# Performance work log

Measured on AMD Instinct MI355X. Metric: run time of the kernel, lower is better.

## Reference

```python
import jax, jax.numpy as jnp
import numpy as np

B, T, D, H = 4, 2048, 1024, 16
DK = D // H

def setup_inputs() -> dict:
    key = jax.random.key(0)
    ks = jax.random.split(key, 5)
    s = 1.0 / np.sqrt(D)
    return {
        "x": jax.random.normal(ks[0], (B, T, D), jnp.float32),
        "Wq": jax.random.normal(ks[1], (D, D), jnp.float32) * s,
        "Wk": jax.random.normal(ks[2], (D, D), jnp.float32) * s,
        "Wv": jax.random.normal(ks[3], (D, D), jnp.float32) * s,
        "Wo": jax.random.normal(ks[4], (D, D), jnp.float32) * s,
    }

def reference(x, Wq, Wk, Wv, Wo):
    # torch Linear: y = x @ W.T (W is [out, in], no bias)
    q = jnp.einsum('btd,ed->bte', x, Wq).reshape(B, T, H, DK).transpose(0, 2, 1, 3)
    k = jnp.einsum('btd,ed->bte', x, Wk).reshape(B, T, H, DK).transpose(0, 2, 1, 3)
    v = jnp.einsum('btd,ed->bte', x, Wv).reshape(B, T, H, DK).transpose(0, 2, 1, 3)
    # scores: [B, H, T, T]
    scores = jnp.einsum('bhqd,bhkd->bhqk', q, k) * (DK ** -0.5)
    causal_mask = jnp.triu(jnp.ones((T, T), dtype=bool), k=1)  # True above diagonal
    scores = jnp.where(causal_mask, -jnp.inf, scores)
    attn = jax.nn.softmax(scores, axis=-1)  # dropout = identity (p=0 / eval)
    ctx = jnp.einsum('bhqk,bhkd->bhqd', attn, v)  # [B, H, T, DK]
    ctx = ctx.transpose(0, 2, 1, 3).reshape(B, T, D)
    out = jnp.einsum('btd,ed->bte', ctx, Wo)
    return out
```

## Files before the change

### kernel.cpp

```cpp
#include <hip/hip_runtime.h>
#include <hip/hip_bf16.h>
#include <stdint.h>

#define BB 4
#define TT 2048
#define DD 1024
#define HH 16
#define DKK 64

typedef unsigned short u16;
typedef unsigned int u32;
typedef __bf16 bf16_t;
typedef bf16_t bf16x8 __attribute__((ext_vector_type(8)));
typedef float f32x4 __attribute__((ext_vector_type(4)));

#if __has_builtin(__builtin_amdgcn_exp2f)
#define EXPW(x) __builtin_amdgcn_exp2f(x)
#define QSCL 0.1803368801111244f
#else
#define EXPW(x) __expf(x)
#define QSCL 0.125f
#endif

__device__ __forceinline__ float bf2f(u16 u) {
    u32 x = ((u32)u) << 16;
    float f;
    __builtin_memcpy(&f, &x, 4);
    return f;
}
__device__ __forceinline__ u16 f2bf(float f) {
    u32 x;
    __builtin_memcpy(&x, &f, 4);
    x += 0x7fffu + ((x >> 16) & 1u);
    return (u16)(x >> 16);
}

__device__ __forceinline__ void gll16(const u16* g, u16* l) {
    __builtin_amdgcn_global_load_lds((const __attribute__((address_space(1))) u32*)g,
                                     (__attribute__((address_space(3))) u32*)l, 16, 0, 0);
}

__global__ void cast_f32_bf16(const float* __restrict__ in, u16* __restrict__ out, int n) {
    int i = (blockIdx.x * blockDim.x + threadIdx.x) * 4;
    int stride = gridDim.x * blockDim.x * 4;
    for (; i < n; i += stride) {
        float4 v = *reinterpret_cast<const float4*>(in + i);
        uint2 pk;
        pk.x = (u32)f2bf(v.x) | ((u32)f2bf(v.y) << 16);
        pk.y = (u32)f2bf(v.z) | ((u32)f2bf(v.w) << 16);
        *reinterpret_cast<uint2*>(out + i) = pk;
    }
}

__global__ void cast_w4(const float* __restrict__ w0, const float* __restrict__ w1,
                        const float* __restrict__ w2, const float* __restrict__ w3,
                        u16* __restrict__ out, int nW) {
    const float* src = (blockIdx.y == 0) ? w0 : (blockIdx.y == 1) ? w1 : (blockIdx.y == 2) ? w2 : w3;
    u16* dst = out + (size_t)blockIdx.y * nW;
    int i = (blockIdx.x * blockDim.x + threadIdx.x) * 4;
    int stride = gridDim.x * blockDim.x * 4;
    for (; i < nW; i += stride) {
        float4 v = *reinterpret_cast<const float4*>(src + i);
        uint2 pk;
        pk.x = (u32)f2bf(v.x) | ((u32)f2bf(v.y) << 16);
        pk.y = (u32)f2bf(v.z) | ((u32)f2bf(v.w) << 16);
        *reinterpret_cast<uint2*>(dst + i) = pk;
    }
}

__device__ __forceinline__ void gemm_128_mainloop(const u16* __restrict__ A,
                                                  const u16* __restrict__ W,
                                                  u16* As, u16* Bs,
                                                  int m0, int n0, f32x4 acc[4][4]) {
    const int tid = threadIdx.x;
    const int lane = tid & 63;
    const int wid = tid >> 6;
    const int wr = (wid >> 1) * 64, wc = (wid & 1) * 64;
    const int l15 = lane & 15, l4 = lane >> 4;

    const f32x4 z4 = {0.f, 0.f, 0.f, 0.f};
#pragma unroll
    for (int i = 0; i < 4; i++)
#pragma unroll
        for (int j = 0; j < 4; j++) acc[i][j] = z4;

    const int r0 = tid >> 2;
    const int c0 = (tid & 3) * 8;

    for (int k0 = 0; k0 < DD; k0 += 32) {
        __syncthreads();
        gll16(A + (m0 + r0) * DD + k0 + c0, As + (wid * 64) * 8);
        gll16(A + (m0 + 64 + r0) * DD + k0 + c0, As + (256 + wid * 64) * 8);
        gll16(W + (n0 + r0) * DD + k0 + c0, Bs + (wid * 64) * 8);
        gll16(W + (n0 + 64 + r0) * DD + k0 + c0, Bs + (256 + wid * 64) * 8);
        asm volatile("s_waitcnt vmcnt(0)" ::: "memory");
        __syncthreads();

        bf16x8 af[4], bfr[4];
#pragma unroll
        for (int mi = 0; mi < 4; mi++)
            af[mi] = *reinterpret_cast<const bf16x8*>(As + (wr + mi * 16 + l15) * 32 + l4 * 8);
#pragma unroll
        for (int ni = 0; ni < 4; ni++)
            bfr[ni] = *reinterpret_cast<const bf16x8*>(Bs + (wc + ni * 16 + l15) * 32 + l4 * 8);
#pragma unroll
        for (int mi = 0; mi < 4; mi++)
#pragma unroll
            for (int ni = 0; ni < 4; ni++)
                acc[mi][ni] =
                    __builtin_amdgcn_mfma_f32_16x16x32_bf16(af[mi], bfr[ni], acc[mi][ni], 0, 0, 0);
    }
}

__global__ __launch_bounds__(256) void gemm_qkv(const u16* __restrict__ xb,
                                                const u16* __restrict__ wq,
                                                const u16* __restrict__ wk,
                                                const u16* __restrict__ wv,
                                                u16* __restrict__ Qo, u16* __restrict__ Ko,
                                                u16* __restrict__ Vto) {
    __shared__ u16 As[128 * 32];
    __shared__ u16 Bs[128 * 32];
    const int z = blockIdx.z;
    const u16* W = (z == 0) ? wq : (z == 1) ? wk : wv;
    u16* dst = (z == 0) ? Qo : (z == 1) ? Ko : Vto;
    const int m0 = blockIdx.x * 128, n0 = blockIdx.y * 128;

    f32x4 acc[4][4];
    gemm_128_mainloop(xb, W, As, Bs, m0, n0, acc);

    const int lane = threadIdx.x & 63, wid = threadIdx.x >> 6;
    const int wr = (wid >> 1) * 64, wc = (wid & 1) * 64;
    const int l15 = lane & 15, l4 = lane >> 4;
#pragma unroll
    for (int mi = 0; mi < 4; mi++)
#pragma unroll
        for (int ni = 0; ni < 4; ni++)
#pragma unroll
            for (int j = 0; j < 4; j++) {
                int m = m0 + wr + mi * 16 + l4 * 4 + j;
                int n = n0 + wc + ni * 16 + l15;
                int b = m >> 11, t = m & (TT - 1);
                int h = n >> 6, dk = n & 63;
                u16 v = f2bf(acc[mi][ni][j]);
                if (z < 2)
                    dst[((b * HH + h) * TT + t) * DKK + dk] = v;
                else
                    dst[((b * HH + h) * DKK + dk) * TT + t] = v;
            }
}

__global__ __launch_bounds__(256) void gemm_out(const u16* __restrict__ ctx,
                                                const u16* __restrict__ wo,
                                                float* __restrict__ out) {
    __shared__ u16 As[128 * 32];
    __shared__ u16 Bs[128 * 32];
    const int m0 = blockIdx.x * 128, n0 = blockIdx.y * 128;
    f32x4 acc[4][4];
    gemm_128_mainloop(ctx, wo, As, Bs, m0, n0, acc);

    const int lane = threadIdx.x & 63, wid = threadIdx.x >> 6;
    const int wr = (wid >> 1) * 64, wc = (wid & 1) * 64;
    const int l15 = lane & 15, l4 = lane >> 4;
#pragma unroll
    for (int mi = 0; mi < 4; mi++)
#pragma unroll
        for (int ni = 0; ni < 4; ni++)
#pragma unroll
            for (int j = 0; j < 4; j++) {
                int m = m0 + wr + mi * 16 + l4 * 4 + j;
                int n = n0 + wc + ni * 16 + l15;
                out[m * DD + n] = acc[mi][ni][j];
            }
}


__device__ __forceinline__ void stage_kv(const u16* __restrict__ Kb, const u16* __restrict__ Vb,
                                         u16* Kd, u16* Vd, int kt, int tid, int wid) {
    int r = tid >> 3, cc = tid & 7;
    int cs = cc ^ (r & 7);
    gll16(Kb + (kt * 64 + r) * DKK + cs * 8, Kd + wid * 64 * 8);
    gll16(Vb + r * TT + kt * 64 + cs * 8, Vd + wid * 64 * 8);
}

__device__ __forceinline__ void load_qfrag16(const u16* Qb, int qbase, int l15, int l4,
                                             bf16x8 qf[2]) {
#pragma unroll
    for (int kc = 0; kc < 2; kc++) {
        const u16* p = Qb + (qbase + l15) * DKK + kc * 32 + l4 * 8;
        union { uint4 u; u16 h[8]; } cv;
        cv.u = *reinterpret_cast<const uint4*>(p);
        u16 o[8];
#pragma unroll
        for (int e = 0; e < 8; e++) o[e] = f2bf(bf2f(cv.h[e]) * QSCL);
        __builtin_memcpy(&qf[kc], o, 16);
    }
}

__device__ __forceinline__ void write_ctx16(u16* __restrict__ ctx, int b, int h, int qbase,
                                            int l15, int l4, const f32x4 acc[4],
                                            const f32x4 lacc) {
#pragma unroll
    for (int j = 0; j < 4; j++) {
        float inv = 1.0f / lacc[j];
        int t = qbase + l4 * 4 + j;
#pragma unroll
        for (int cf = 0; cf < 4; cf++) {
            int dk = cf * 16 + l15;
            ctx[((size_t)(b * TT + t)) * DD + h * 64 + dk] = f2bf(acc[cf][j] * inv);
        }
    }
}

__device__ __forceinline__ void attn_side(const bf16x8 qf[2], f32x4 acc[4], f32x4& lacc,
                                          const char* Kl, const char* Vl, char* Pw,
                                          bf16x8 onef, int l15, int l4,
                                          bool domask, int kt, int qbase) {
    const f32x4 z4 = {0.f, 0.f, 0.f, 0.f};
    f32x4 s[4];
#pragma unroll
    for (int cf = 0; cf < 4; cf++) s[cf] = z4;

#pragma unroll
    for (int kc = 0; kc < 2; kc++) {
#pragma unroll
        for (int cf = 0; cf < 4; cf++) {
            int kr = cf * 16 + l15;
            int cw = (l4 + kc * 4) ^ (kr & 7);
            bf16x8 kf = *reinterpret_cast<const bf16x8*>(Kl + kr * 128 + cw * 16);
            s[cf] = __builtin_amdgcn_mfma_f32_16x16x32_bf16(qf[kc], kf, s[cf], 0, 0, 0);
        }
    }

#pragma unroll
    for (int cf = 0; cf < 4; cf++)
#pragma unroll
        for (int j = 0; j < 4; j++) {
            float v = s[cf][j];
            if (domask) {
                int kk = kt * 64 + cf * 16 + l15;
                int qq = qbase + l4 * 4 + j;
                if (kk > qq) v = -__builtin_huge_valf();
            }
            float p = EXPW(v);
            int r = l4 * 4 + j;
            int col = cf * 16 + l15;
            int byte = r * 128 + (((col >> 3) ^ (r & 7)) << 4) + (col & 7) * 2;
            *reinterpret_cast<u16*>(Pw + byte) = f2bf(p);
        }

    asm volatile("s_waitcnt lgkmcnt(0)" ::: "memory");
    __builtin_amdgcn_sched_barrier(0);

#pragma unroll
    for (int kc = 0; kc < 2; kc++) {
        int cwp = (l4 + kc * 4) ^ (l15 & 7);
        bf16x8 pa = *reinterpret_cast<const bf16x8*>(Pw + l15 * 128 + cwp * 16);
#pragma unroll
        for (int cf = 0; cf < 4; cf++) {
            int vr = cf * 16 + l15;
            int vw = (l4 + kc * 4) ^ (vr & 7);
            bf16x8 vf = *reinterpret_cast<const bf16x8*>(Vl + vr * 128 + vw * 16);
            acc[cf] = __builtin_amdgcn_mfma_f32_16x16x32_bf16(pa, vf, acc[cf], 0, 0, 0);
        }
        lacc = __builtin_amdgcn_mfma_f32_16x16x32_bf16(pa, onef, lacc, 0, 0, 0);
    }
}

__global__ __launch_bounds__(512, 2) void attn_fwd(const u16* __restrict__ Qg,
                                                   const u16* __restrict__ Kg,
                                                   const u16* __restrict__ Vtg,
                                                   u16* __restrict__ ctx) {
    __shared__ u16 Kld[2][64 * 64];
    __shared__ u16 Vld[2][64 * 64];
    __shared__ u16 Pld[8][2][16 * 64];

    const int tid = threadIdx.x;
    const int lane = tid & 63, wid = tid >> 6;
    const int l15 = lane & 15, l4 = lane >> 4;
    const int bh = blockIdx.y;
    const int jA = blockIdx.x, jB = 15 - jA;
    const int qbaseA = jA * 128 + wid * 16;
    const int qbaseB = jB * 128 + wid * 16;
    const int nA = 2 * jA + 1 + (wid >> 2);
    const int nB = 2 * jB + 1 + (wid >> 2);
    const int nkt = 2 * jB + 2;

    const u16* Qb = Qg + (size_t)bh * TT * DKK;
    const u16* Kb = Kg + (size_t)bh * TT * DKK;
    const u16* Vb = Vtg + (size_t)bh * DKK * TT;

    bf16x8 qfA[2], qfB[2];
    load_qfrag16(Qb, qbaseA, l15, l4, qfA);
    load_qfrag16(Qb, qbaseB, l15, l4, qfB);

    bf16x8 onef;
    {
        union { bf16x8 v; u16 h[8]; } o;
#pragma unroll
        for (int e = 0; e < 8; e++) o.h[e] = 0x3F80;
        onef = o.v;
    }

    f32x4 accA[4], accB[4], laccA, laccB;
    const f32x4 z4 = {0.f, 0.f, 0.f, 0.f};
#pragma unroll
    for (int j = 0; j < 4; j++) { accA[j] = z4; accB[j] = z4; }
    laccA = z4; laccB = z4;

    char* PwA = reinterpret_cast<char*>(&Pld[wid][0][0]);
    char* PwB = reinterpret_cast<char*>(&Pld[wid][1][0]);

    stage_kv(Kb, Vb, Kld[0], Vld[0], 0, tid, wid);

    for (int kt = 0; kt < nkt; kt++) {
        if (kt + 1 < nkt) {
            stage_kv(Kb, Vb, Kld[(kt + 1) & 1], Vld[(kt + 1) & 1], kt + 1, tid, wid);
            asm volatile("s_waitcnt vmcnt(2)" ::: "memory");
        } else {
            asm volatile("s_waitcnt vmcnt(0)" ::: "memory");
        }
        __syncthreads();

        const char* Kl = reinterpret_cast<const char*>(Kld[kt & 1]);
        const char* Vl = reinterpret_cast<const char*>(Vld[kt & 1]);

        if (kt < nA)
            attn_side(qfA, accA, laccA, Kl, Vl, PwA, onef, l15, l4, kt == nA - 1, kt, qbaseA);
        if (kt < nB)
            attn_side(qfB, accB, laccB, Kl, Vl, PwB, onef, l15, l4, kt == nB - 1, kt, qbaseB);
        __syncthreads();
    }

    const int b = bh >> 4, h = bh & 15;
    write_ctx16(ctx, b, h, qbaseA, l15, l4, accA, laccA);
    write_ctx16(ctx, b, h, qbaseB, l15, l4, accB, laccB);
}

extern "C" void kernel_launch(void* const* d_in, const int* in_sizes, int n_in,
                              void* d_out, int out_size, void* d_ws, size_t ws_size,
                              hipStream_t stream) {
    const float* x = (const float*)d_in[0];
    const float* Wq = (const float*)d_in[1];
    const float* Wk = (const float*)d_in[2];
    const float* Wv = (const float*)d_in[3];
    const float* Wo = (const float*)d_in[4];

    const int nX = BB * TT * DD;
    const int nW = DD * DD;
    const int nQ = BB * HH * TT * DKK;

    u16* xb = (u16*)d_ws;
    u16* wqb = xb + nX;
    u16* wkb = wqb + nW;
    u16* wvb = wkb + nW;
    u16* wob = wvb + nW;
    u16* Qb = wob + nW;
    u16* Kb = Qb + nQ;
    u16* Vtb = Kb + nQ;
    u16* ctxb = Vtb + nQ;

    cast_f32_bf16<<<4096, 256, 0, stream>>>(x, xb, nX);
    cast_w4<<<dim3(1024, 4), 256, 0, stream>>>(Wq, Wk, Wv, Wo, wqb, nW);

    gemm_qkv<<<dim3((BB * TT) / 128, DD / 128, 3), 256, 0, stream>>>(xb, wqb, wkb, wvb, Qb, Kb, Vtb);

    attn_fwd<<<dim3(8, BB * HH), 512, 0, stream>>>(Qb, Kb, Vtb, ctxb);

    gemm_out<<<dim3((BB * TT) / 128, DD / 128), 256, 0, stream>>>(ctxb, wob, (float*)d_out);
}
```

Before: 217.8 us.

## Drop LDS K/V staging in attention; read K/V directly from global per wave

```diff
diff --git a/kernel.cpp b/kernel.cpp
--- a/kernel.cpp
+++ b/kernel.cpp
@@ -174,16 +174,15 @@
 }
 
 
-__device__ __forceinline__ void stage_kv(const u16* __restrict__ Kb, const u16* __restrict__ Vb,
-                                         u16* Kd, u16* Vd, int kt, int tid, int wid) {
-    int r = tid >> 3, cc = tid & 7;
-    int cs = cc ^ (r & 7);
-    gll16(Kb + (kt * 64 + r) * DKK + cs * 8, Kd + wid * 64 * 8);
-    gll16(Vb + r * TT + kt * 64 + cs * 8, Vd + wid * 64 * 8);
-}
-
-__device__ __forceinline__ void load_qfrag16(const u16* Qb, int qbase, int l15, int l4,
-                                             bf16x8 qf[2]) {
+__device__ __forceinline__ void attn_one(const u16* __restrict__ Qb,
+                                         const u16* __restrict__ Kb,
+                                         const u16* __restrict__ Vb,
+                                         u16* __restrict__ ctx, int b, int h,
+                                         int qbase, char* Pw, int l15, int l4,
+                                         bf16x8 onef) {
+    const f32x4 z4 = {0.f, 0.f, 0.f, 0.f};
+
+    bf16x8 qf[2];
 #pragma unroll
     for (int kc = 0; kc < 2; kc++) {
         const u16* p = Qb + (qbase + l15) * DKK + kc * 32 + l4 * 8;
@@ -194,11 +193,64 @@
         for (int e = 0; e < 8; e++) o[e] = f2bf(bf2f(cv.h[e]) * QSCL);
         __builtin_memcpy(&qf[kc], o, 16);
     }
-}
-
-__device__ __forceinline__ void write_ctx16(u16* __restrict__ ctx, int b, int h, int qbase,
-                                            int l15, int l4, const f32x4 acc[4],
-                                            const f32x4 lacc) {
+
+    f32x4 acc[4], lacc = z4;
+#pragma unroll
+    for (int j = 0; j < 4; j++) acc[j] = z4;
+
+    const int n = ((qbase + 15) >> 6) + 1;
+
+    for (int kt = 0; kt < n; kt++) {
+        const u16* Kt = Kb + kt * 64 * DKK;
+
+        f32x4 s[4];
+#pragma unroll
+        for (int cf = 0; cf < 4; cf++) s[cf] = z4;
+#pragma unroll
+        for (int kc = 0; kc < 2; kc++) {
+#pragma unroll
+            for (int cf = 0; cf < 4; cf++) {
+                bf16x8 kf = *reinterpret_cast<const bf16x8*>(
+                    Kt + (cf * 16 + l15) * DKK + kc * 32 + l4 * 8);
+                s[cf] = __builtin_amdgcn_mfma_f32_16x16x32_bf16(qf[kc], kf, s[cf], 0, 0, 0);
+            }
+        }
+
+        const bool domask = (kt == n - 1);
+#pragma unroll
+        for (int cf = 0; cf < 4; cf++)
+#pragma unroll
+            for (int j = 0; j < 4; j++) {
+                float v = s[cf][j];
+                if (domask) {
+                    int kk = kt * 64 + cf * 16 + l15;
+                    int qq = qbase + l4 * 4 + j;
+                    if (kk > qq) v = -__builtin_huge_valf();
+                }
+                float p = EXPW(v);
+                int r = l4 * 4 + j;
+                int col = cf * 16 + l15;
+                int byte = r * 128 + (((col >> 3) ^ (r & 7)) << 4) + (col & 7) * 2;
+                *reinterpret_cast<u16*>(Pw + byte) = f2bf(p);
+            }
+
+        asm volatile("s_waitcnt lgkmcnt(0)" ::: "memory");
+        __builtin_amdgcn_sched_barrier(0);
+
+#pragma unroll
+        for (int kc = 0; kc < 2; kc++) {
+            int cwp = (l4 + kc * 4) ^ (l15 & 7);
+            bf16x8 pa = *reinterpret_cast<const bf16x8*>(Pw + l15 * 128 + cwp * 16);
+#pragma unroll
+            for (int cf = 0; cf < 4; cf++) {
+                bf16x8 vf = *reinterpret_cast<const bf16x8*>(
+                    Vb + (cf * 16 + l15) * TT + kt * 64 + kc * 32 + l4 * 8);
+                acc[cf] = __builtin_amdgcn_mfma_f32_16x16x32_bf16(pa, vf, acc[cf], 0, 0, 0);
+            }
+            lacc = __builtin_amdgcn_mfma_f32_16x16x32_bf16(pa, onef, lacc, 0, 0, 0);
+        }
+    }
+
 #pragma unroll
     for (int j = 0; j < 4; j++) {
         float inv = 1.0f / lacc[j];
@@ -211,88 +263,25 @@
     }
 }
 
-__device__ __forceinline__ void attn_side(const bf16x8 qf[2], f32x4 acc[4], f32x4& lacc,
-                                          const char* Kl, const char* Vl, char* Pw,
-                                          bf16x8 onef, int l15, int l4,
-                                          bool domask, int kt, int qbase) {
-    const f32x4 z4 = {0.f, 0.f, 0.f, 0.f};
-    f32x4 s[4];
-#pragma unroll
-    for (int cf = 0; cf < 4; cf++) s[cf] = z4;
-
-#pragma unroll
-    for (int kc = 0; kc < 2; kc++) {
-#pragma unroll
-        for (int cf = 0; cf < 4; cf++) {
-            int kr = cf * 16 + l15;
-            int cw = (l4 + kc * 4) ^ (kr & 7);
-            bf16x8 kf = *reinterpret_cast<const bf16x8*>(Kl + kr * 128 + cw * 16);
-            s[cf] = __builtin_amdgcn_mfma_f32_16x16x32_bf16(qf[kc], kf, s[cf], 0, 0, 0);
-        }
-    }
-
-#pragma unroll
-    for (int cf = 0; cf < 4; cf++)
-#pragma unroll
-        for (int j = 0; j < 4; j++) {
-            float v = s[cf][j];
-            if (domask) {
-                int kk = kt * 64 + cf * 16 + l15;
-                int qq = qbase + l4 * 4 + j;
-                if (kk > qq) v = -__builtin_huge_valf();
-            }
-            float p = EXPW(v);
-            int r = l4 * 4 + j;
-            int col = cf * 16 + l15;
-            int byte = r * 128 + (((col >> 3) ^ (r & 7)) << 4) + (col & 7) * 2;
-            *reinterpret_cast<u16*>(Pw + byte) = f2bf(p);
-        }
-
-    asm volatile("s_waitcnt lgkmcnt(0)" ::: "memory");
-    __builtin_amdgcn_sched_barrier(0);
-
-#pragma unroll
-    for (int kc = 0; kc < 2; kc++) {
-        int cwp = (l4 + kc * 4) ^ (l15 & 7);
-        bf16x8 pa = *reinterpret_cast<const bf16x8*>(Pw + l15 * 128 + cwp * 16);
-#pragma unroll
-        for (int cf = 0; cf < 4; cf++) {
-            int vr = cf * 16 + l15;
-            int vw = (l4 + kc * 4) ^ (vr & 7);
-            bf16x8 vf = *reinterpret_cast<const bf16x8*>(Vl + vr * 128 + vw * 16);
-            acc[cf] = __builtin_amdgcn_mfma_f32_16x16x32_bf16(pa, vf, acc[cf], 0, 0, 0);
-        }
-        lacc = __builtin_amdgcn_mfma_f32_16x16x32_bf16(pa, onef, lacc, 0, 0, 0);
-    }
-}
-
-__global__ __launch_bounds__(512, 2) void attn_fwd(const u16* __restrict__ Qg,
+__global__ __launch_bounds__(256, 4) void attn_fwd(const u16* __restrict__ Qg,
                                                    const u16* __restrict__ Kg,
                                                    const u16* __restrict__ Vtg,
                                                    u16* __restrict__ ctx) {
-    __shared__ u16 Kld[2][64 * 64];
-    __shared__ u16 Vld[2][64 * 64];
-    __shared__ u16 Pld[8][2][16 * 64];
+    __shared__ u16 Pld[4][16 * 64];
 
     const int tid = threadIdx.x;
     const int lane = tid & 63, wid = tid >> 6;
     const int l15 = lane & 15, l4 = lane >> 4;
     const int bh = blockIdx.y;
-    const int jA = blockIdx.x, jB = 15 - jA;
-    const int qbaseA = jA * 128 + wid * 16;
-    const int qbaseB = jB * 128 + wid * 16;
-    const int nA = 2 * jA + 1 + (wid >> 2);
-    const int nB = 2 * jB + 1 + (wid >> 2);
-    const int nkt = 2 * jB + 2;
+    const int pair = blockIdx.x >> 1, half = blockIdx.x & 1;
+    const int jA = pair, jB = 15 - pair;
+    const int qbaseA = jA * 128 + half * 64 + wid * 16;
+    const int qbaseB = jB * 128 + half * 64 + wid * 16;
 
     const u16* Qb = Qg + (size_t)bh * TT * DKK;
     const u16* Kb = Kg + (size_t)bh * TT * DKK;
     const u16* Vb = Vtg + (size_t)bh * DKK * TT;
 
-    bf16x8 qfA[2], qfB[2];
-    load_qfrag16(Qb, qbaseA, l15, l4, qfA);
-    load_qfrag16(Qb, qbaseB, l15, l4, qfB);
-
     bf16x8 onef;
     {
         union { bf16x8 v; u16 h[8]; } o;
@@ -301,39 +290,11 @@
         onef = o.v;
     }
 
-    f32x4 accA[4], accB[4], laccA, laccB;
-    const f32x4 z4 = {0.f, 0.f, 0.f, 0.f};
-#pragma unroll
-    for (int j = 0; j < 4; j++) { accA[j] = z4; accB[j] = z4; }
-    laccA = z4; laccB = z4;
-
-    char* PwA = reinterpret_cast<char*>(&Pld[wid][0][0]);
-    char* PwB = reinterpret_cast<char*>(&Pld[wid][1][0]);
-
-    stage_kv(Kb, Vb, Kld[0], Vld[0], 0, tid, wid);
-
-    for (int kt = 0; kt < nkt; kt++) {
-        if (kt + 1 < nkt) {
-            stage_kv(Kb, Vb, Kld[(kt + 1) & 1], Vld[(kt + 1) & 1], kt + 1, tid, wid);
-            asm volatile("s_waitcnt vmcnt(2)" ::: "memory");
-        } else {
-            asm volatile("s_waitcnt vmcnt(0)" ::: "memory");
-        }
-        __syncthreads();
-
-        const char* Kl = reinterpret_cast<const char*>(Kld[kt & 1]);
-        const char* Vl = reinterpret_cast<const char*>(Vld[kt & 1]);
-
-        if (kt < nA)
-            attn_side(qfA, accA, laccA, Kl, Vl, PwA, onef, l15, l4, kt == nA - 1, kt, qbaseA);
-        if (kt < nB)
-            attn_side(qfB, accB, laccB, Kl, Vl, PwB, onef, l15, l4, kt == nB - 1, kt, qbaseB);
-        __syncthreads();
-    }
-
+    char* Pw = reinterpret_cast<char*>(&Pld[wid][0]);
     const int b = bh >> 4, h = bh & 15;
-    write_ctx16(ctx, b, h, qbaseA, l15, l4, accA, laccA);
-    write_ctx16(ctx, b, h, qbaseB, l15, l4, accB, laccB);
+
+    attn_one(Qb, Kb, Vb, ctx, b, h, qbaseA, Pw, l15, l4, onef);
+    attn_one(Qb, Kb, Vb, ctx, b, h, qbaseB, Pw, l15, l4, onef);
 }
 
 extern "C" void kernel_launch(void* const* d_in, const int* in_sizes, int n_in,
@@ -364,7 +325,7 @@
 
     gemm_qkv<<<dim3((BB * TT) / 128, DD / 128, 3), 256, 0, stream>>>(xb, wqb, wkb, wvb, Qb, Kb, Vtb);
 
-    attn_fwd<<<dim3(8, BB * HH), 512, 0, stream>>>(Qb, Kb, Vtb, ctxb);
+    attn_fwd<<<dim3(16, BB * HH), 256, 0, stream>>>(Qb, Kb, Vtb, ctxb);
 
     gemm_out<<<dim3((BB * TT) / 128, DD / 128), 256, 0, stream>>>(ctxb, wob, (float*)d_out);
 }
```

New measurement: 359.5 us. 65.0% more time.
